# Kernel tuning notes

Measured on AMD Instinct MI355X. Metric: run time of the kernel, lower is better.

## Reference

```python
import jax, jax.numpy as jnp
import numpy as np

EPS = 1e-3  # keras LayerNormalization default epsilon


def _layernorm(x, gamma, beta):
    mu = jnp.mean(x, axis=-1, keepdims=True)
    var = jnp.mean(jnp.square(x - mu), axis=-1, keepdims=True)
    return (x - mu) * jax.lax.rsqrt(var + EPS) * gamma + beta


def setup_inputs() -> dict:
    key = jax.random.key(0)
    B, T, D, H = 8, 2048, 192, 3
    KD = D           # TalkingHeadsAttention(key_dim=dim, value_dim=dim)
    HID = 4 * D      # mlp_ratio = 4.0
    ks = jax.random.split(key, 12)
    s_in = 0.02
    inp = {
        "x": jax.random.normal(ks[0], (B, T, D), jnp.float32),
        # norm1 / norm2
        "gamma1": jnp.ones((D,), jnp.float32),
        "beta1": jnp.zeros((D,), jnp.float32),
        "gamma2": jnp.ones((D,), jnp.float32),
        "beta2": jnp.zeros((D,), jnp.float32),
        # attention projections (qkv_bias=False -> no biases)
        "wq": jax.random.normal(ks[1], (D, H, KD), jnp.float32) * s_in,
        "wk": jax.random.normal(ks[2], (D, H, KD), jnp.float32) * s_in,
        "wv": jax.random.normal(ks[3], (D, H, KD), jnp.float32) * s_in,
        "wo": jax.random.normal(ks[4], (H, KD, D), jnp.float32) * s_in,
        # talking-heads mixing matrices [H, H]
        "pre_w": jnp.eye(H, dtype=jnp.float32) + jax.random.normal(ks[5], (H, H), jnp.float32) * 0.02,
        "post_w": jnp.eye(H, dtype=jnp.float32) + jax.random.normal(ks[6], (H, H), jnp.float32) * 0.02,
        # MLP (bias=True)
        "w1": jax.random.normal(ks[7], (D, HID), jnp.float32) * s_in,
        "b1": jnp.zeros((HID,), jnp.float32),
        "w2": jax.random.normal(ks[8], (HID, D), jnp.float32) * s_in,
        "b2": jnp.zeros((D,), jnp.float32),
    }
    return inp


def reference(x, gamma1, beta1, gamma2, beta2, wq, wk, wv, wo, pre_w, post_w, w1, b1, w2, b2):
    KD = wq.shape[-1]
    # --- pre-norm + talking-heads attention ---
    n = _layernorm(x, gamma1, beta1)                      # [B,T,D]
    q = jnp.einsum("btd,dhk->bthk", n, wq)               # [B,T,H,KD]
    k = jnp.einsum("bsd,dhk->bshk", n, wk)
    v = jnp.einsum("bsd,dhk->bshk", n, wv)
    scores = jnp.einsum("bthk,bshk->bhts", q, k) / jnp.sqrt(jnp.asarray(KD, x.dtype))
    scores = jnp.einsum("bhts,hg->bgts", scores, pre_w)   # pre-softmax head mix
    probs = jax.nn.softmax(scores, axis=-1)
    probs = jnp.einsum("bhts,hg->bgts", probs, post_w)    # post-softmax head mix
    ctx = jnp.einsum("bhts,bshk->bthk", probs, v)         # [B,T,H,KD]
    attn_out = jnp.einsum("bthk,hkd->btd", ctx, wo)       # [B,T,D]
    x = x + attn_out                                      # ls1/drop_path1 are Identity
    # --- pre-norm + MLP ---
    n2 = _layernorm(x, gamma2, beta2)
    h = jax.nn.gelu(n2 @ w1 + b1, approximate=False)      # keras gelu = exact erf
    mlp_out = h @ w2 + b2
    return x + mlp_out
```

## Files before the change

### kernel.cpp

```cpp
#include <hip/hip_runtime.h>
#include <hip/hip_bf16.h>

typedef __hip_bfloat16 bf16;
typedef unsigned char u8;
typedef __attribute__((ext_vector_type(8))) __bf16 bf16x8;
typedef __attribute__((ext_vector_type(4))) float f32x4;
typedef __attribute__((ext_vector_type(2))) float f32x2;

__device__ __forceinline__ void gld_lds16(const void* g, void* l) {
  __builtin_amdgcn_global_load_lds((const __attribute__((address_space(1))) void*)g,
                                   (__attribute__((address_space(3))) void*)l, 16, 0, 0);
}
__device__ __forceinline__ u8 f2e4m3(float v) {
  return (u8)(__builtin_amdgcn_cvt_pk_fp8_f32(v, 0.f, 0, false) & 0xff);
}
__device__ __forceinline__ f32x2 pk_mul(f32x2 a, f32x2 b) {
  f32x2 d;
  asm("v_pk_mul_f32 %0, %1, %2" : "=v"(d) : "v"(a), "v"(b));
  return d;
}
__device__ __forceinline__ f32x2 pk_fma(f32x2 a, f32x2 b, f32x2 c) {
  f32x2 d;
  asm("v_pk_fma_f32 %0, %1, %2, %3" : "=v"(d) : "v"(a), "v"(b), "v"(c));
  return d;
}

__global__ __launch_bounds__(256) void setup_k(
    const float* __restrict__ x, const float* __restrict__ gamma1, const float* __restrict__ beta1,
    const float* __restrict__ wq, const float* __restrict__ wk,
    const float* __restrict__ wv, const float* __restrict__ wo,
    const float* __restrict__ post_w, const float* __restrict__ w1, const float* __restrict__ w2,
    bf16* __restrict__ nb, bf16* __restrict__ WqkvT,
    bf16* __restrict__ w1f, bf16* __restrict__ w2f)
{
  const int bid = blockIdx.x;
  if (bid < 432) {
    const int j = bid * 256 + threadIdx.x;
    const int dd = j % 192;
    const int r = j / 192;
    const int h = r / 192, din = r % 192;
    float acc = 0.f;
    #pragma unroll
    for (int g2 = 0; g2 < 3; ++g2) {
      const float pw = post_w[h*3 + g2];
      const float* wvp = wv + (size_t)din*576 + g2*192;
      const float* wop = wo + (size_t)(g2*192)*192 + dd;
      float s0 = 0.f, s1 = 0.f, s2 = 0.f, s3 = 0.f;
      for (int kd = 0; kd < 192; kd += 4) {
        s0 += wvp[kd]     * wop[(size_t)kd*192];
        s1 += wvp[kd + 1] * wop[(size_t)(kd + 1)*192];
        s2 += wvp[kd + 2] * wop[(size_t)(kd + 2)*192];
        s3 += wvp[kd + 3] * wop[(size_t)(kd + 3)*192];
      }
      acc += pw * ((s0 + s1) + (s2 + s3));
    }
    WqkvT[(size_t)(1152 + h*192 + dd)*192 + din] = __float2bfloat16(acc);
    return;
  }
  if (bid < 2448) {
    int i = (bid - 432) * 256 + threadIdx.x;
    if (i < 221184) {
      int n = i / 192, d = i % 192;
      int sel = n / 576, c = n % 576, h = c / 192, kd = c % 192;
      const float* w = (sel == 0) ? wq : wk;
      WqkvT[i] = __float2bfloat16(w[(d*3 + h)*192 + kd]);
      return;
    }
    i -= 221184;
    if (i < 147456) {
      int j = i / 192, k = i % 192;
      int c = j >> 6, jc = j & 63, jb = jc >> 4, j15 = jc & 15;
      int kq = k >> 5, sl = (k & 31) >> 3, e7 = k & 7;
      w1f[(size_t)(((c*6 + kq)*4 + jb)*512) + (j15 + (sl << 4))*8 + e7] =
          __float2bfloat16(w1[(size_t)k*768 + j]);
      return;
    }
    i -= 147456;
    {
      int j = i / 192, d = i % 192;
      int c = j >> 6, ks = (j >> 5) & 1, l4 = (j >> 3) & 3, e = j & 7;
      int dn = d >> 4, l15 = d & 15;
      w2f[(size_t)((((c*2 + ks)*12 + dn)*64) + l4*16 + l15)*8 + e] =
          __float2bfloat16(w2[(size_t)j*192 + d]);
    }
    return;
  }
  {
    int row = (bid - 2448) * 4 + (threadIdx.x >> 6);
    int lane = threadIdx.x & 63;
    const float* xr = x + (size_t)row * 192;
    float v0 = xr[lane], v1 = xr[lane + 64], v2 = xr[lane + 128];
    float s = v0 + v1 + v2;
    #pragma unroll
    for (int o = 32; o; o >>= 1) s += __shfl_xor(s, o);
    float mu = s * (1.f / 192.f);
    float d0 = v0 - mu, d1 = v1 - mu, d2 = v2 - mu;
    float q = d0*d0 + d1*d1 + d2*d2;
    #pragma unroll
    for (int o = 32; o; o >>= 1) q += __shfl_xor(q, o);
    float rs = rsqrtf(q * (1.f / 192.f) + 1e-3f);
    bf16* orow = nb + (size_t)row * 192;
    orow[lane]       = __float2bfloat16(d0*rs*gamma1[lane]       + beta1[lane]);
    orow[lane + 64]  = __float2bfloat16(d1*rs*gamma1[lane + 64]  + beta1[lane + 64]);
    orow[lane + 128] = __float2bfloat16(d2*rs*gamma1[lane + 128] + beta1[lane + 128]);
  }
}

__global__ __launch_bounds__(256) void gemm_qkv(
    const bf16* __restrict__ A, const bf16* __restrict__ BT,
    u8* __restrict__ q_out, u8* __restrict__ k_out, u8* __restrict__ mt_out)
{
  const int K = 192;
  const int tid = threadIdx.x, lane = tid & 63, wid = tid >> 6;
  const int l15 = lane & 15, l4 = lane >> 4;
  const int wm = wid >> 1, wn = wid & 1;
  const int row0 = blockIdx.y * 128, col0 = blockIdx.x * 64;
  const int sel0 = col0 / 576;
  __shared__ __align__(16) bf16 As[2][128 * 32];
  __shared__ __align__(16) bf16 Bs[2][64 * 32];
  f32x4 acc[4][2] = {};

#define STAGE(buf_, kt_) do { \
    const bf16* Ab_ = A + (size_t)row0 * K + (kt_) * 32; \
    int c0_ = tid, r0_ = c0_ >> 2, cc0_ = (c0_ & 3) << 3; \
    gld_lds16(Ab_ + (size_t)r0_ * K + cc0_, &As[buf_][c0_ * 8]); \
    int c1_ = tid + 256, r1_ = c1_ >> 2, cc1_ = (c1_ & 3) << 3; \
    gld_lds16(Ab_ + (size_t)r1_ * K + cc1_, &As[buf_][c1_ * 8]); \
    const bf16* Bb_ = BT + (size_t)col0 * K + (kt_) * 32; \
    gld_lds16(Bb_ + (size_t)(tid >> 2) * K + ((tid & 3) << 3), &Bs[buf_][tid * 8]); \
  } while (0)

  STAGE(0, 0);
  for (int kt = 0; kt < 6; ++kt) {
    __syncthreads();
    const int buf = kt & 1;
    if (kt + 1 < 6) STAGE(buf ^ 1, kt + 1);
    const int koff = l4 * 8;
    bf16x8 af[4], bfr[2];
    #pragma unroll
    for (int m = 0; m < 4; ++m)
      af[m] = *(const bf16x8*)&As[buf][(wm*64 + m*16 + l15)*32 + koff];
    #pragma unroll
    for (int n = 0; n < 2; ++n)
      bfr[n] = *(const bf16x8*)&Bs[buf][(wn*32 + n*16 + l15)*32 + koff];
    if (sel0 < 2) {
      #pragma unroll
      for (int m = 0; m < 4; ++m)
        #pragma unroll
        for (int n = 0; n < 2; ++n)
          acc[m][n] = __builtin_amdgcn_mfma_f32_16x16x32_bf16(bfr[n], af[m], acc[m][n], 0, 0, 0);
    } else {
      #pragma unroll
      for (int m = 0; m < 4; ++m)
        #pragma unroll
        for (int n = 0; n < 2; ++n)
          acc[m][n] = __builtin_amdgcn_mfma_f32_16x16x32_bf16(af[m], bfr[n], acc[m][n], 0, 0, 0);
    }
  }
#undef STAGE

  if (sel0 < 2) {
    u8* dst = (sel0 == 0) ? q_out : k_out;
    #pragma unroll
    for (int m = 0; m < 4; ++m) {
      const int t = row0 + wm*64 + m*16 + l15;
      const int b = t >> 11, t2 = t & 2047;
      #pragma unroll
      for (int n = 0; n < 2; ++n) {
        const int c2 = (col0 - sel0*576) + wn*32 + n*16 + l4*4;
        const int h = c2 / 192, kd = c2 % 192;
        int pk = __builtin_amdgcn_cvt_pk_fp8_f32(acc[m][n][0], acc[m][n][1], 0, false);
        pk = __builtin_amdgcn_cvt_pk_fp8_f32(acc[m][n][2], acc[m][n][3], pk, true);
        const size_t fo = ((((size_t)b*64 + (t2>>5))*3 + h)*6 + (kd>>5))*1024
                        + (((t2>>4)&1))*512
                        + (((t2&15) + (((kd>>3)&3)<<4))<<3) + (kd&7);
        *(unsigned*)&dst[fo] = (unsigned)pk;
      }
    }
  } else {
    const int rbase = row0 + wm * 64;
    const int cbase = col0 + wn * 32;
    #pragma unroll
    for (int m = 0; m < 4; ++m) {
      #pragma unroll
      for (int n = 0; n < 2; ++n) {
        const int col = cbase + n*16 + l15;
        const int rtop = rbase + m*16 + (l4 << 2);
        const int b = rtop >> 11, t_ = rtop & 2047;
        const int c2 = col % 576;
        const int h = c2 / 192, kd = c2 % 192;
        int pk = __builtin_amdgcn_cvt_pk_fp8_f32(acc[m][n][0], acc[m][n][1], 0, false);
        pk = __builtin_amdgcn_cvt_pk_fp8_f32(acc[m][n][2], acc[m][n][3], pk, true);
        const size_t fo = ((((size_t)b*64 + (t_>>5))*3 + h)*12 + (kd>>4))*512
                        + (((kd&15) + (((t_>>3)&3)<<4))<<3) + (t_&4);
        *(unsigned*)&mt_out[fo] = (unsigned)pk;
      }
    }
  }
}

__global__ __launch_bounds__(256, 2) void attn_k(
    const u8* __restrict__ q, const u8* __restrict__ kf,
    const u8* __restrict__ MT, const float* __restrict__ pre_w,
    const float* __restrict__ x, const float* __restrict__ gamma2,
    const float* __restrict__ beta2, const bf16* __restrict__ w1f,
    const bf16* __restrict__ w2f, const float* __restrict__ b1,
    const float* __restrict__ b2, float* __restrict__ out)
{
  const int tid = threadIdx.x, lane = tid & 63, wv = tid >> 6;
  const int l15 = lane & 15, l4 = lane >> 4;
  const int tq = wv & 1, sq = wv >> 1;
  const int bid = blockIdx.x;
  const int b = bid & 7;
  const int tt = bid >> 3;
  const int t0 = tt * 32;

  __shared__ __align__(16) u8 S[69632];
  __shared__ float rlPart[2][3][32];
  __shared__ float lnS[4][32][2];
  u8* KsP = S;
  u8* PsP = S + 36864;
  bf16* N2 = (bf16*)S;
  bf16* BsP = (bf16*)(S + 12288);
  bf16* HfP = (bf16*)(S + 61440);

  const u8* qfb = q + ((size_t)b*64 + tt) * 18432;
  long qf[3][6];
  #pragma unroll
  for (int h = 0; h < 3; ++h)
    #pragma unroll
    for (int kq = 0; kq < 6; ++kq)
      qf[h][kq] = *(const long*)(qfb + ((h*6 + kq)*2 + tq)*512 + lane*8);

  f32x2 pwf2[9];
  #pragma unroll
  for (int i = 0; i < 9; ++i) {
    const float v = pre_w[i] * 0.07216878364870323f * 1.44269504088896f;
    pwf2[i][0] = v; pwf2[i][1] = v;
  }

  f32x4 acc[3][2][3] = {};
  float sgacc[3] = {0.f, 0.f, 0.f};
  const int trow = tq*16 + l15;
  const int psw = (l15 >> 2) & 3;
  const int pwr = (((sq*2 + (l4 >> 1)) ^ psw) << 3) + ((l4 & 1) << 2);
  const int prd = (l4 ^ psw) << 3;

  const u8* kfb = kf + (size_t)b * 64 * 18432;
  const u8* mtb = MT + (size_t)b * 64 * 18432;

#define STAGEK(buf_, st_) do { \
    const u8* kb_ = kfb + (size_t)(st_) * 18432; \
    _Pragma("unroll") \
    for (int i_ = 0; i_ < 5; ++i_) { \
      const int L_ = i_ * 256 + tid; \
      if (L_ < 1152) gld_lds16(kb_ + L_*16, KsP + (buf_)*18432 + L_*16); \
    } \
  } while (0)

#define LOADMF(MF_, st_) do { \
    const u8* mb_ = mtb + (size_t)(st_) * 18432 + wv*3*512 + lane*8; \
    _Pragma("unroll") \
    for (int g_ = 0; g_ < 3; ++g_) \
      _Pragma("unroll") \
      for (int n_ = 0; n_ < 3; ++n_) \
        MF_[g_][n_] = *(const long*)(mb_ + (g_*12 + n_)*512); \
  } while (0)

#define PV(stm1_, MF_) do { \
    const int bp_ = (stm1_) & 1; \
    __builtin_amdgcn_s_setprio(1); \
    _Pragma("unroll") \
    for (int g_ = 0; g_ < 3; ++g_) \
      _Pragma("unroll") \
      for (int m_ = 0; m_ < 2; ++m_) { \
        const long pf_ = *(const long*)(PsP + bp_*3072 + g_*1024 + (m_*16 + l15)*32 + prd); \
        _Pragma("unroll") \
        for (int n_ = 0; n_ < 3; ++n_) \
          acc[g_][m_][n_] = __builtin_amdgcn_mfma_f32_16x16x32_fp8_fp8(pf_, MF_[g_][n_], acc[g_][m_][n_], 0, 0, 0); \
      } \
    __builtin_amdgcn_s_setprio(0); \
  } while (0)

#define QKSM(st_) do { \
    const int bq_ = (st_) & 1; \
    f32x4 sacc0 = {}, sacc1 = {}, sacc2 = {}; \
    __builtin_amdgcn_s_setprio(1); \
    _Pragma("unroll") \
    for (int kq_ = 0; kq_ < 6; ++kq_) { \
      const long kf0_ = *(const long*)(KsP + bq_*18432 + (((0*6 + kq_)*2 + sq)*512) + lane*8); \
      sacc0 = __builtin_amdgcn_mfma_f32_16x16x32_fp8_fp8(kf0_, qf[0][kq_], sacc0, 0, 0, 0); \
      const long kf1_ = *(const long*)(KsP + bq_*18432 + (((1*6 + kq_)*2 + sq)*512) + lane*8); \
      sacc1 = __builtin_amdgcn_mfma_f32_16x16x32_fp8_fp8(kf1_, qf[1][kq_], sacc1, 0, 0, 0); \
      const long kf2_ = *(const long*)(KsP + bq_*18432 + (((2*6 + kq_)*2 + sq)*512) + lane*8); \
      sacc2 = __builtin_amdgcn_mfma_f32_16x16x32_fp8_fp8(kf2_, qf[2][kq_], sacc2, 0, 0, 0); \
    } \
    __builtin_amdgcn_s_setprio(0); \
    f32x2 p0a = {sacc0[0], sacc0[1]}, p0b = {sacc0[2], sacc0[3]}; \
    f32x2 p1a = {sacc1[0], sacc1[1]}, p1b = {sacc1[2], sacc1[3]}; \
    f32x2 p2a = {sacc2[0], sacc2[1]}, p2b = {sacc2[2], sacc2[3]}; \
    _Pragma("unroll") \
    for (int g_ = 0; g_ < 3; ++g_) { \
      f32x2 va = pk_mul(p0a, pwf2[g_]); \
      va = pk_fma(p1a, pwf2[3+g_], va); \
      va = pk_fma(p2a, pwf2[6+g_], va); \
      f32x2 vb = pk_mul(p0b, pwf2[g_]); \
      vb = pk_fma(p1b, pwf2[3+g_], vb); \
      vb = pk_fma(p2b, pwf2[6+g_], vb); \
      float e0_ = exp2f(va[0]), e1_ = exp2f(va[1]); \
      float e2_ = exp2f(vb[0]), e3_ = exp2f(vb[1]); \
      sgacc[g_] += (e0_ + e1_) + (e2_ + e3_); \
      int pk_ = __builtin_amdgcn_cvt_pk_fp8_f32(e0_, e1_, 0, false); \
      pk_ = __builtin_amdgcn_cvt_pk_fp8_f32(e2_, e3_, pk_, true); \
      *(unsigned*)(PsP + bq_*3072 + g_*1024 + trow*32 + pwr) = (unsigned)pk_; \
    } \
  } while (0)

#define STAGEB(buf_, c_) do { \
    const u8* wsrc_ = (const u8*)w1f + (size_t)(c_) * 24576; \
    _Pragma("unroll") \
    for (int i_ = 0; i_ < 6; ++i_) { \
      const int L_ = i_ * 256 + tid; \
      gld_lds16(wsrc_ + L_*16, (u8*)BsP + (buf_)*24576 + L_*16); \
    } \
  } while (0)

#define LOADWF(WF_, c_) do { \
    _Pragma("unroll") \
    for (int n_ = 0; n_ < 3; ++n_) \
      _Pragma("unroll") \
      for (int ks_ = 0; ks_ < 2; ++ks_) \
        WF_[n_][ks_] = *(const bf16x8*)(w2f + (size_t)(((((c_)*2 + ks_)*12) + wv*3 + n_)*64 + lane)*8); \
  } while (0)

  const int wmm = wv >> 1, wnn = wv & 1;

#define MGEMM1(c_) do { \
    f32x4 sacc[2] = {}; \
    _Pragma("unroll") \
    for (int kq_ = 0; kq_ < 6; ++kq_) { \
      const bf16x8 af_ = *(const bf16x8*)&N2[((kq_*2 + wmm)*512) + lane*8]; \
      _Pragma("unroll") \
      for (int n_ = 0; n_ < 2; ++n_) { \
        const bf16x8 bfr_ = *(const bf16x8*)&BsP[((c_)&1)*12288 + ((kq_*4 + wnn*2 + n_)*512) + lane*8]; \
        sacc[n_] = __builtin_amdgcn_mfma_f32_16x16x32_bf16(af_, bfr_, sacc[n_], 0, 0, 0); \
      } \
    } \
    _Pragma("unroll") \
    for (int n_ = 0; n_ < 2; ++n_) { \
      const int jc_ = wnn*32 + n_*16 + l15; \
      const float bv_ = b1[(c_)*64 + jc_]; \
      const int sl_ = (jc_ & 31) >> 3, e7_ = jc_ & 7; \
      _Pragma("unroll") \
      for (int jr_ = 0; jr_ < 4; ++jr_) { \
        const int r15_ = l4*4 + jr_; \
        const float u_ = sacc[n_][jr_] + bv_; \
        const float g_ = 0.5f * u_ * (1.f + erff(u_ * 0.70710678118654752f)); \
        HfP[((c_)&1)*2048 + ((wnn*2 + wmm)*512) + ((r15_ + (sl_ << 4)) << 3) + e7_] = __float2bfloat16(g_); \
      } \
    } \
  } while (0)

#define MGEMM2(WF_, hbuf_) do { \
    _Pragma("unroll") \
    for (int ks_ = 0; ks_ < 2; ++ks_) { \
      bf16x8 ha_[2]; \
      _Pragma("unroll") \
      for (int m_ = 0; m_ < 2; ++m_) \
        ha_[m_] = *(const bf16x8*)&HfP[(hbuf_)*2048 + ((ks_*2 + m_)*512) + lane*8]; \
      _Pragma("unroll") \
      for (int m_ = 0; m_ < 2; ++m_) \
        _Pragma("unroll") \
        for (int n_ = 0; n_ < 3; ++n_) \
          macc[m_][n_] = __builtin_amdgcn_mfma_f32_16x16x32_bf16(ha_[m_], WF_[n_][ks_], macc[m_][n_], 0, 0, 0); \
    } \
  } while (0)

  long mfA[3][3], mfB[3][3];

  STAGEK(0, 0);
  __syncthreads();
  STAGEK(1, 1);
  LOADMF(mfA, 0);
  QKSM(0);
  for (int st = 1; st < 63; st += 2) {
    __syncthreads();
    STAGEK((st + 1) & 1, st + 1);
    LOADMF(mfB, st);
    PV(st - 1, mfA);
    QKSM(st);
    __syncthreads();
    if (st + 2 < 64) STAGEK((st + 2) & 1, st + 2);
    LOADMF(mfA, st + 1);
    PV(st, mfB);
    QKSM(st + 1);
  }
  __syncthreads();
  LOADMF(mfB, 63);
  PV(62, mfA);
  QKSM(63);
  __syncthreads();
  PV(63, mfB);
  STAGEB(0, 0);
  #pragma unroll
  for (int g = 0; g < 3; ++g) {
    float s = sgacc[g];
    s += __shfl_xor(s, 16);
    s += __shfl_xor(s, 32);
    if (l4 == 0) rlPart[sq][g][trow] = s;
  }
  float xv[2][3][4];
  #pragma unroll
  for (int m = 0; m < 2; ++m)
    #pragma unroll
    for (int n = 0; n < 3; ++n) {
      const int d = wv*48 + n*16 + l15;
      #pragma unroll
      for (int j = 0; j < 4; ++j)
        xv[m][n][j] = x[((size_t)b*2048 + t0 + m*16 + l4*4 + j)*192 + d];
    }
  __syncthreads();

  float ovv[2][3][4];
  #pragma unroll
  for (int m = 0; m < 2; ++m) {
    #pragma unroll
    for (int j = 0; j < 4; ++j) {
      const int row = m*16 + l4*4 + j;
      float rlv[3];
      #pragma unroll
      for (int g = 0; g < 3; ++g)
        rlv[g] = 1.f / (rlPart[0][g][row] + rlPart[1][g][row]);
      float s = 0.f, ss = 0.f;
      #pragma unroll
      for (int n = 0; n < 3; ++n) {
        const float ov = xv[m][n][j] + rlv[0]*acc[0][m][n][j] + rlv[1]*acc[1][m][n][j]
                                     + rlv[2]*acc[2][m][n][j];
        ovv[m][n][j] = ov;
        s += ov; ss += ov*ov;
      }
      #pragma unroll
      for (int o = 1; o < 16; o <<= 1) { s += __shfl_xor(s, o); ss += __shfl_xor(ss, o); }
      if (l15 == 0) { lnS[wv][row][0] = s; lnS[wv][row][1] = ss; }
    }
  }
  __syncthreads();

  {
    float gmL[3], btL[3];
    #pragma unroll
    for (int n = 0; n < 3; ++n) {
      const int d = wv*48 + n*16 + l15;
      gmL[n] = gamma2[d]; btL[n] = beta2[d];
    }
    #pragma unroll
    for (int m = 0; m < 2; ++m) {
      #pragma unroll
      for (int j = 0; j < 4; ++j) {
        const int row = m*16 + l4*4 + j;
        const float ts  = lnS[0][row][0] + lnS[1][row][0] + lnS[2][row][0] + lnS[3][row][0];
        const float tss = lnS[0][row][1] + lnS[1][row][1] + lnS[2][row][1] + lnS[3][row][1];
        const float mu = ts * (1.f / 192.f);
        const float rs = rsqrtf(tss * (1.f / 192.f) - mu*mu + 1e-3f);
        #pragma unroll
        for (int n = 0; n < 3; ++n) {
          const int d = wv*48 + n*16 + l15;
          N2[(((d>>5)*2 + m)*512) + (((row&15) + (((d&31)>>3)<<4))<<3) + (d&7)] =
              __float2bfloat16((ovv[m][n][j] - mu) * rs * gmL[n] + btL[n]);
        }
      }
    }
  }
  __syncthreads();

  f32x4 macc[2][3] = {};
  bf16x8 wfA[3][2], wfB[3][2];

  STAGEB(1, 1);
  LOADWF(wfA, 0);
  MGEMM1(0);
  __syncthreads();
  for (int c = 1; c < 11; c += 2) {
    STAGEB((c + 1) & 1, c + 1);
    LOADWF(wfB, c);
    MGEMM2(wfA, (c - 1) & 1);
    MGEMM1(c);
    __syncthreads();
    if (c + 2 < 12) STAGEB((c + 2) & 1, c + 2);
    LOADWF(wfA, c + 1);
    MGEMM2(wfB, c & 1);
    MGEMM1(c + 1);
    __syncthreads();
  }
  LOADWF(wfB, 11);
  MGEMM2(wfA, 0);
  MGEMM1(11);
  __syncthreads();
  MGEMM2(wfB, 1);

  #pragma unroll
  for (int n = 0; n < 3; ++n) {
    const int d = wv*48 + n*16 + l15;
    const float b2v = b2[d];
    #pragma unroll
    for (int m = 0; m < 2; ++m) {
      #pragma unroll
      for (int jr = 0; jr < 4; ++jr) {
        const int row = m*16 + l4*4 + jr;
        const size_t idx = ((size_t)b*2048 + t0 + row)*192 + d;
        out[idx] = ovv[m][n][jr] + macc[m][n][jr] + b2v;
      }
    }
  }
#undef STAGEK
#undef LOADMF
#undef PV
#undef QKSM
#undef STAGEB
#undef LOADWF
#undef MGEMM1
#undef MGEMM2
}

extern "C" void kernel_launch(void* const* d_in, const int* in_sizes, int n_in,
                              void* d_out, int out_size, void* d_ws, size_t ws_size,
                              hipStream_t stream)
{
  (void)in_sizes; (void)n_in; (void)out_size; (void)ws_size;
  const float* x      = (const float*)d_in[0];
  const float* gamma1 = (const float*)d_in[1];
  const float* beta1  = (const float*)d_in[2];
  const float* gamma2 = (const float*)d_in[3];
  const float* beta2  = (const float*)d_in[4];
  const float* wq     = (const float*)d_in[5];
  const float* wk     = (const float*)d_in[6];
  const float* wv     = (const float*)d_in[7];
  const float* wo     = (const float*)d_in[8];
  const float* pre_w  = (const float*)d_in[9];
  const float* post_w = (const float*)d_in[10];
  const float* w1     = (const float*)d_in[11];
  const float* b1     = (const float*)d_in[12];
  const float* w2     = (const float*)d_in[13];
  const float* b2     = (const float*)d_in[14];
  float* out = (float*)d_out;

  uint8_t* base = (uint8_t*)d_ws;
  size_t off = 0;
  auto alloc = [&](size_t bytes) {
    uint8_t* r = base + off; off += (bytes + 255) & ~(size_t)255; return r;
  };
  bf16* nb      = (bf16*)alloc((size_t)16384 * 192 * 2);
  u8*   qb      = (u8*)alloc((size_t)9437184);
  u8*   kb      = (u8*)alloc((size_t)9437184);
  u8*   MTslab  = (u8*)alloc((size_t)9437184);
  bf16* WqkvT   = (bf16*)alloc((size_t)331776 * 2);
  bf16* w1f     = (bf16*)alloc((size_t)147456 * 2);
  bf16* w2f     = (bf16*)alloc((size_t)147456 * 2);

  setup_k<<<6544, 256, 0, stream>>>(x, gamma1, beta1, wq, wk, wv, wo, post_w, w1, w2,
                                    nb, WqkvT, w1f, w2f);
  gemm_qkv<<<dim3(27, 128, 1), 256, 0, stream>>>(nb, WqkvT, qb, kb, MTslab);
  attn_k<<<512, 256, 0, stream>>>(qb, kb, MTslab, pre_w, x, gamma2, beta2,
                                  w1f, w2f, b1, b2, out);
}
```

Before: 161.4 us.

## Split attention over key halves and combine partials in separate MLP kernel

Splits the attention kernel's key sequence into two halves, launching 1024 blocks instead of 512. Each block writes unnormalized bf16 partial context and partial softmax denominators to the workspace. A new combine kernel sums the two partials, normalizes, adds the residual and runs LayerNorm plus the MLP. This aims to raise occupancy and fill the GPU better, at the cost of extra global traffic for partials, an extra launch and bf16 rounding of the partial accumulators. The softmax has no max subtraction, so summing the partials is exact apart from that rounding.

Result: slower. 175.8 us (+8.9%).

```diff
diff --git a/kernel.cpp b/kernel.cpp
--- a/kernel.cpp
+++ b/kernel.cpp
@@ -10,9 +10,6 @@
 __device__ __forceinline__ void gld_lds16(const void* g, void* l) {
   __builtin_amdgcn_global_load_lds((const __attribute__((address_space(1))) void*)g,
                                    (__attribute__((address_space(3))) void*)l, 16, 0, 0);
-}
-__device__ __forceinline__ u8 f2e4m3(float v) {
-  return (u8)(__builtin_amdgcn_cvt_pk_fp8_f32(v, 0.f, 0, false) & 0xff);
 }
 __device__ __forceinline__ f32x2 pk_mul(f32x2 a, f32x2 b) {
   f32x2 d;
@@ -202,27 +199,20 @@
 __global__ __launch_bounds__(256, 2) void attn_k(
     const u8* __restrict__ q, const u8* __restrict__ kf,
     const u8* __restrict__ MT, const float* __restrict__ pre_w,
-    const float* __restrict__ x, const float* __restrict__ gamma2,
-    const float* __restrict__ beta2, const bf16* __restrict__ w1f,
-    const bf16* __restrict__ w2f, const float* __restrict__ b1,
-    const float* __restrict__ b2, float* __restrict__ out)
+    bf16* __restrict__ Opart, float* __restrict__ Lpart)
 {
   const int tid = threadIdx.x, lane = tid & 63, wv = tid >> 6;
   const int l15 = lane & 15, l4 = lane >> 4;
   const int tq = wv & 1, sq = wv >> 1;
   const int bid = blockIdx.x;
   const int b = bid & 7;
-  const int tt = bid >> 3;
-  const int t0 = tt * 32;
-
-  __shared__ __align__(16) u8 S[69632];
+  const int tt = (bid >> 3) >> 1;
+  const int sh = (bid >> 3) & 1;
+
+  __shared__ __align__(16) u8 S[43008];
   __shared__ float rlPart[2][3][32];
-  __shared__ float lnS[4][32][2];
   u8* KsP = S;
   u8* PsP = S + 36864;
-  bf16* N2 = (bf16*)S;
-  bf16* BsP = (bf16*)(S + 12288);
-  bf16* HfP = (bf16*)(S + 61440);
 
   const u8* qfb = q + ((size_t)b*64 + tt) * 18432;
   long qf[3][6];
@@ -246,8 +236,8 @@
   const int pwr = (((sq*2 + (l4 >> 1)) ^ psw) << 3) + ((l4 & 1) << 2);
   const int prd = (l4 ^ psw) << 3;
 
-  const u8* kfb = kf + (size_t)b * 64 * 18432;
-  const u8* mtb = MT + (size_t)b * 64 * 18432;
+  const u8* kfb = kf + ((size_t)b*64 + sh*32) * 18432;
+  const u8* mtb = MT + ((size_t)b*64 + sh*32) * 18432;
 
 #define STAGEK(buf_, st_) do { \
     const u8* kb_ = kfb + (size_t)(st_) * 18432; \
@@ -316,6 +306,88 @@
     } \
   } while (0)
 
+  long mfA[3][3], mfB[3][3];
+
+  STAGEK(0, 0);
+  __syncthreads();
+  STAGEK(1, 1);
+  LOADMF(mfA, 0);
+  QKSM(0);
+  for (int st = 1; st < 31; st += 2) {
+    __syncthreads();
+    STAGEK((st + 1) & 1, st + 1);
+    LOADMF(mfB, st);
+    PV(st - 1, mfA);
+    QKSM(st);
+    __syncthreads();
+    if (st + 2 < 32) STAGEK((st + 2) & 1, st + 2);
+    LOADMF(mfA, st + 1);
+    PV(st, mfB);
+    QKSM(st + 1);
+  }
+  __syncthreads();
+  LOADMF(mfB, 31);
+  PV(30, mfA);
+  QKSM(31);
+  __syncthreads();
+  PV(31, mfB);
+  #pragma unroll
+  for (int g = 0; g < 3; ++g) {
+    float s = sgacc[g];
+    s += __shfl_xor(s, 16);
+    s += __shfl_xor(s, 32);
+    if (l4 == 0) rlPart[sq][g][trow] = s;
+  }
+  __syncthreads();
+
+  if (tid < 96) {
+    const int g = tid >> 5, row = tid & 31;
+    Lpart[(size_t)bid*96 + g*32 + row] = rlPart[0][g][row] + rlPart[1][g][row];
+  }
+  bf16* op = Opart + (size_t)bid * 3 * 32 * 192;
+  #pragma unroll
+  for (int g = 0; g < 3; ++g)
+    #pragma unroll
+    for (int m = 0; m < 2; ++m)
+      #pragma unroll
+      for (int n = 0; n < 3; ++n) {
+        const int d = wv*48 + n*16 + l15;
+        #pragma unroll
+        for (int j = 0; j < 4; ++j)
+          op[(g*32 + m*16 + l4*4 + j)*192 + d] = __float2bfloat16(acc[g][m][n][j]);
+      }
+#undef STAGEK
+#undef LOADMF
+#undef PV
+#undef QKSM
+}
+
+__global__ __launch_bounds__(256, 2) void comb_k(
+    const bf16* __restrict__ Opart, const float* __restrict__ Lpart,
+    const float* __restrict__ x, const float* __restrict__ gamma2,
+    const float* __restrict__ beta2, const bf16* __restrict__ w1f,
+    const bf16* __restrict__ w2f, const float* __restrict__ b1,
+    const float* __restrict__ b2, float* __restrict__ out)
+{
+  const int tid = threadIdx.x, lane = tid & 63, wv = tid >> 6;
+  const int l15 = lane & 15, l4 = lane >> 4;
+  const int cid = blockIdx.x;
+  const int b = cid & 7;
+  const int tt = cid >> 3;
+  const int t0 = tt * 32;
+
+  __shared__ __align__(16) u8 S[69632];
+  __shared__ float Ls[3][32];
+  __shared__ float lnS[4][32][2];
+  bf16* N2 = (bf16*)S;
+  bf16* BsP = (bf16*)(S + 12288);
+  bf16* HfP = (bf16*)(S + 61440);
+
+  const int bid0 = ((tt*2 + 0) << 3) | b;
+  const int bid1 = ((tt*2 + 1) << 3) | b;
+  const bf16* op0 = Opart + (size_t)bid0 * 3 * 32 * 192;
+  const bf16* op1 = Opart + (size_t)bid1 * 3 * 32 * 192;
+
 #define STAGEB(buf_, c_) do { \
     const u8* wsrc_ = (const u8*)w1f + (size_t)(c_) * 24576; \
     _Pragma("unroll") \
@@ -376,49 +448,10 @@
     } \
   } while (0)
 
-  long mfA[3][3], mfB[3][3];
-
-  STAGEK(0, 0);
-  __syncthreads();
-  STAGEK(1, 1);
-  LOADMF(mfA, 0);
-  QKSM(0);
-  for (int st = 1; st < 63; st += 2) {
-    __syncthreads();
-    STAGEK((st + 1) & 1, st + 1);
-    LOADMF(mfB, st);
-    PV(st - 1, mfA);
-    QKSM(st);
-    __syncthreads();
-    if (st + 2 < 64) STAGEK((st + 2) & 1, st + 2);
-    LOADMF(mfA, st + 1);
-    PV(st, mfB);
-    QKSM(st + 1);
-  }
-  __syncthreads();
-  LOADMF(mfB, 63);
-  PV(62, mfA);
-  QKSM(63);
-  __syncthreads();
-  PV(63, mfB);
-  STAGEB(0, 0);
-  #pragma unroll
-  for (int g = 0; g < 3; ++g) {
-    float s = sgacc[g];
-    s += __shfl_xor(s, 16);
-    s += __shfl_xor(s, 32);
-    if (l4 == 0) rlPart[sq][g][trow] = s;
-  }
-  float xv[2][3][4];
-  #pragma unroll
-  for (int m = 0; m < 2; ++m)
-    #pragma unroll
-    for (int n = 0; n < 3; ++n) {
-      const int d = wv*48 + n*16 + l15;
-      #pragma unroll
-      for (int j = 0; j < 4; ++j)
-        xv[m][n][j] = x[((size_t)b*2048 + t0 + m*16 + l4*4 + j)*192 + d];
-    }
+  if (tid < 96) {
+    const int g = tid >> 5, row = tid & 31;
+    Ls[g][row] = Lpart[(size_t)bid0*96 + g*32 + row] + Lpart[(size_t)bid1*96 + g*32 + row];
+  }
   __syncthreads();
 
   float ovv[2][3][4];
@@ -429,13 +462,17 @@
       const int row = m*16 + l4*4 + j;
       float rlv[3];
       #pragma unroll
-      for (int g = 0; g < 3; ++g)
-        rlv[g] = 1.f / (rlPart[0][g][row] + rlPart[1][g][row]);
+      for (int g = 0; g < 3; ++g) rlv[g] = 1.f / Ls[g][row];
       float s = 0.f, ss = 0.f;
       #pragma unroll
       for (int n = 0; n < 3; ++n) {
-        const float ov = xv[m][n][j] + rlv[0]*acc[0][m][n][j] + rlv[1]*acc[1][m][n][j]
-                                     + rlv[2]*acc[2][m][n][j];
+        const int d = wv*48 + n*16 + l15;
+        const size_t pidx = (size_t)row*192 + d;
+        float ov = x[((size_t)b*2048 + t0 + row)*192 + d];
+        #pragma unroll
+        for (int g = 0; g < 3; ++g)
+          ov += rlv[g] * (__bfloat162float(op0[g*32*192 + pidx]) +
+                          __bfloat162float(op1[g*32*192 + pidx]));
         ovv[m][n][j] = ov;
         s += ov; ss += ov*ov;
       }
@@ -444,6 +481,7 @@
       if (l15 == 0) { lnS[wv][row][0] = s; lnS[wv][row][1] = ss; }
     }
   }
+  STAGEB(0, 0);
   __syncthreads();
 
   {
@@ -475,7 +513,6 @@
 
   f32x4 macc[2][3] = {};
   bf16x8 wfA[3][2], wfB[3][2];
-
   STAGEB(1, 1);
   LOADWF(wfA, 0);
   MGEMM1(0);
@@ -512,10 +549,6 @@
       }
     }
   }
-#undef STAGEK
-#undef LOADMF
-#undef PV
-#undef QKSM
 #undef STAGEB
 #undef LOADWF
 #undef MGEMM1
@@ -556,10 +589,13 @@
   bf16* WqkvT   = (bf16*)alloc((size_t)331776 * 2);
   bf16* w1f     = (bf16*)alloc((size_t)147456 * 2);
   bf16* w2f     = (bf16*)alloc((size_t)147456 * 2);
+  bf16* Opart   = (bf16*)alloc((size_t)1024 * 3 * 32 * 192 * 2);
+  float* Lpart  = (float*)alloc((size_t)1024 * 96 * 4);
 
   setup_k<<<6544, 256, 0, stream>>>(x, gamma1, beta1, wq, wk, wv, wo, post_w, w1, w2,
                                     nb, WqkvT, w1f, w2f);
   gemm_qkv<<<dim3(27, 128, 1), 256, 0, stream>>>(nb, WqkvT, qb, kb, MTslab);
-  attn_k<<<512, 256, 0, stream>>>(qb, kb, MTslab, pre_w, x, gamma2, beta2,
+  attn_k<<<1024, 256, 0, stream>>>(qb, kb, MTslab, pre_w, Opart, Lpart);
+  comb_k<<<512, 256, 0, stream>>>(Opart, Lpart, x, gamma2, beta2,
                                   w1f, w2f, b1, b2, out);
 }
```
